# Performance work log

Measured on AMD Instinct MI355X. Metric: run time of the kernel, lower is better.

The kernel has to match this reference:

```python
import jax, jax.numpy as jnp
import numpy as np

MARGIN = 1.0


def _rand_offdiag(key, n):
    # uniform random index j != k for each row k (replaces Python random.choice)
    j = jax.random.randint(key, (n,), 0, n - 1)
    return j + (j >= jnp.arange(n)).astype(j.dtype)


def _semi_hard_margin_loss(logits, j_rand, j_fallback, margin):
    # logits: [N, N]; anchor for row k is logits[k, k]
    n = logits.shape[0]
    rows = jnp.arange(n)
    anchor = jnp.diagonal(logits)                      # [N]
    # term 1: random imposter, hinge at 0 (loss added only when diff > 0)
    imp1 = logits[rows, j_rand]
    d1 = jnp.maximum(imp1 - anchor + margin, 0.0)
    # term 2: semi-hard imposter = max over entries strictly below the anchor
    neg_inf = jnp.finfo(logits.dtype).min
    mask = logits < anchor[:, None]                    # diagonal never True
    cand_max = jnp.max(jnp.where(mask, logits, neg_inf), axis=1)
    has_cand = jnp.any(mask, axis=1)
    imp2 = jnp.where(has_cand, cand_max, logits[rows, j_fallback])
    d2 = jnp.maximum(imp2 - anchor + margin, 0.0)
    return jnp.mean(d1 + d2)


def setup_inputs() -> dict:
    key = jax.random.key(0)
    kx, ky = jax.random.split(key)
    x = jax.random.normal(kx, (4096, 1024), dtype=jnp.float32)
    y = jax.random.normal(ky, (4096, 1024), dtype=jnp.float32)
    return {"x": x, "y": y}


def reference(x, y):
    logits = jnp.matmul(x, y.T)                        # [N, N]
    n = logits.shape[0]
    k1, k2, k3, k4 = jax.random.split(jax.random.key(42), 4)
    loss = (_semi_hard_margin_loss(logits, _rand_offdiag(k1, n), _rand_offdiag(k2, n), MARGIN)
            + _semi_hard_margin_loss(logits.T, _rand_offdiag(k3, n), _rand_offdiag(k4, n), MARGIN))
    return loss
```

## Files before the change

### kernel.cpp

```cpp
#include <hip/hip_runtime.h>
#include <stdint.h>
#include <stddef.h>

#define NN 4096
#define KK 1024
#define SPAN 4095u

typedef unsigned short ushort_t;
typedef __attribute__((ext_vector_type(8))) short short8v;
typedef __attribute__((ext_vector_type(4))) float f32x4;

__host__ __device__ inline void tf2x32(uint32_t k0, uint32_t k1,
                                       uint32_t x0, uint32_t x1,
                                       uint32_t* o0, uint32_t* o1) {
  uint32_t ks2 = k0 ^ k1 ^ 0x1BD11BDAu;
  uint32_t v0 = x0 + k0;
  uint32_t v1 = x1 + k1;
#define TF_ROT(x, r) (((x) << (r)) | ((x) >> (32 - (r))))
#define TF_RND(r) do { v0 += v1; v1 = TF_ROT(v1, r); v1 ^= v0; } while (0)
  TF_RND(13); TF_RND(15); TF_RND(26); TF_RND(6);
  v0 += k1;  v1 += ks2 + 1u;
  TF_RND(17); TF_RND(29); TF_RND(16); TF_RND(24);
  v0 += ks2; v1 += k0 + 2u;
  TF_RND(13); TF_RND(15); TF_RND(26); TF_RND(6);
  v0 += k0;  v1 += k1 + 3u;
  TF_RND(17); TF_RND(29); TF_RND(16); TF_RND(24);
  v0 += k1;  v1 += ks2 + 4u;
  TF_RND(13); TF_RND(15); TF_RND(26); TF_RND(6);
  v0 += ks2; v1 += k0 + 5u;
#undef TF_RND
#undef TF_ROT
  *o0 = v0; *o1 = v1;
}

__device__ inline uint32_t rb32(uint32_t ka, uint32_t kb, uint32_t i) {
  uint32_t a, b;
  tf2x32(ka, kb, 0u, i, &a, &b);
  return a ^ b;
}

__device__ inline uint32_t fenc(float f) {
  uint32_t b = __float_as_uint(f);
  return (b & 0x80000000u) ? ~b : (b | 0x80000000u);
}
__device__ inline float fdec(uint32_t e) {
  uint32_t b = (e & 0x80000000u) ? (e & 0x7FFFFFFFu) : ~e;
  return __uint_as_float(b);
}

__device__ inline ushort_t bf16rne(float f) {
  uint32_t u = __float_as_uint(f);
  return (ushort_t)((u + 0x7FFFu + ((u >> 16) & 1u)) >> 16);
}

__device__ inline void glds16(const void* g, void* l) {
  __builtin_amdgcn_global_load_lds((const __attribute__((address_space(1))) void*)g,
                                   (__attribute__((address_space(3))) void*)l, 16, 0, 0);
}

template <int N> __device__ __forceinline__ void vmwait() {
  if constexpr (N == 8)      asm volatile("s_waitcnt vmcnt(8)" ::: "memory");
  else if constexpr (N == 4) asm volatile("s_waitcnt vmcnt(4)" ::: "memory");
  else                       asm volatile("s_waitcnt vmcnt(0)" ::: "memory");
}

__global__ __launch_bounds__(256) void k_prep(
    const float4* __restrict__ X, const float4* __restrict__ Y,
    ushort4* __restrict__ Xb, ushort4* __restrict__ Yb,
    uint32_t* __restrict__ rowmax, uint32_t* __restrict__ colmax) {
  const int b = blockIdx.x, tid = threadIdx.x;
  if (b < 16) rowmax[b * 256 + tid] = 0u;
  else if (b < 32) colmax[(b - 16) * 256 + tid] = 0u;
  const float4* src = (b < 2048) ? X : Y;
  ushort4* dst = (b < 2048) ? Xb : Yb;
  const int n4 = NN * KK / 4;
  for (int i = (b & 2047) * 256 + tid; i < n4; i += 2048 * 256) {
    float4 v = src[i];
    ushort4 o;
    o.x = bf16rne(v.x); o.y = bf16rne(v.y); o.z = bf16rne(v.z); o.w = bf16rne(v.w);
    dst[i] = o;
  }
}

__global__ __launch_bounds__(256) void k_dots(
    const float* __restrict__ X, const float* __restrict__ Y,
    uint32_t s0a, uint32_t s0b, uint32_t s1a, uint32_t s1b,
    uint32_t s2a, uint32_t s2b, uint32_t s3a, uint32_t s3b,
    float* __restrict__ anchor, float* __restrict__ irr, float* __restrict__ irf,
    float* __restrict__ icr, float* __restrict__ icf) {
  const int wid = threadIdx.x >> 6;
  const int lane = threadIdx.x & 63;
  const int row = blockIdx.x * 4 + wid;

  int jl = 0;
  if (lane < 4) {
    uint32_t ka = (lane == 0) ? s0a : (lane == 1) ? s1a : (lane == 2) ? s2a : s3a;
    uint32_t kb = (lane == 0) ? s0b : (lane == 1) ? s1b : (lane == 2) ? s2b : s3b;
    uint32_t k1a, k1b, k2a, k2b;
    tf2x32(ka, kb, 0u, 0u, &k1a, &k1b);
    tf2x32(ka, kb, 0u, 1u, &k2a, &k2b);
    uint32_t hi = rb32(k1a, k1b, (uint32_t)row);
    uint32_t lo = rb32(k2a, k2b, (uint32_t)row);
    uint32_t off = ((hi % SPAN) * 256u + (lo % SPAN)) % SPAN;
    int j = (int)off;
    jl = j + ((j >= row) ? 1 : 0);
  }
  const int j1r = __shfl(jl, 0), j1f = __shfl(jl, 1);
  const int j2r = __shfl(jl, 2), j2f = __shfl(jl, 3);

  const float4* xk = (const float4*)(X + (size_t)row * KK);
  const float4* yk = (const float4*)(Y + (size_t)row * KK);
  const float4* y1 = (const float4*)(Y + (size_t)j1r * KK);
  const float4* y2 = (const float4*)(Y + (size_t)j1f * KK);
  const float4* x1 = (const float4*)(X + (size_t)j2r * KK);
  const float4* x2 = (const float4*)(X + (size_t)j2f * KK);
  float sa = 0.f, s1 = 0.f, s2 = 0.f, s3 = 0.f, s4 = 0.f;
  for (int t = lane; t < KK / 4; t += 64) {
    float4 xv = xk[t], yv = yk[t], a1 = y1[t], a2 = y2[t], b1 = x1[t], b2 = x2[t];
    sa = fmaf(xv.x, yv.x, fmaf(xv.y, yv.y, fmaf(xv.z, yv.z, fmaf(xv.w, yv.w, sa))));
    s1 = fmaf(xv.x, a1.x, fmaf(xv.y, a1.y, fmaf(xv.z, a1.z, fmaf(xv.w, a1.w, s1))));
    s2 = fmaf(xv.x, a2.x, fmaf(xv.y, a2.y, fmaf(xv.z, a2.z, fmaf(xv.w, a2.w, s2))));
    s3 = fmaf(b1.x, yv.x, fmaf(b1.y, yv.y, fmaf(b1.z, yv.z, fmaf(b1.w, yv.w, s3))));
    s4 = fmaf(b2.x, yv.x, fmaf(b2.y, yv.y, fmaf(b2.z, yv.z, fmaf(b2.w, yv.w, s4))));
  }
  for (int m = 32; m >= 1; m >>= 1) {
    sa += __shfl_xor(sa, m);
    s1 += __shfl_xor(s1, m);
    s2 += __shfl_xor(s2, m);
    s3 += __shfl_xor(s3, m);
    s4 += __shfl_xor(s4, m);
  }
  if (lane == 0) {
    anchor[row] = sa; irr[row] = s1; irf[row] = s2; icr[row] = s3; icf[row] = s4;
  }
}

#define TBM 256
#define TBK 32
#define TNT (KK / TBK)

__global__ __launch_bounds__(512, 2) void k_gemm256(
    const ushort_t* __restrict__ A, const ushort_t* __restrict__ B,
    const float* __restrict__ anchor,
    uint32_t* __restrict__ rowmax, uint32_t* __restrict__ colmax) {
  __shared__ ushort_t Als[4][TBM * TBK];
  __shared__ ushort_t Bls[4][TBM * TBK];

  const int tid = threadIdx.x;
  const int lane = tid & 63;
  const int w = tid >> 6;
  const int wr = w >> 2, wc = w & 3;
  const int l15 = lane & 15, l4 = lane >> 4;

  const int swz = (blockIdx.x & 7) * 32 + (blockIdx.x >> 3);
  const int bi = swz >> 4, bj = swz & 15;

  const int sr = tid >> 2;
  const int ps = (tid & 3) ^ ((sr >> 1) & 3);
  const ushort_t* Ab0 = A + (size_t)(bi * TBM + sr) * KK + ps * 8;
  const ushort_t* Ab1 = Ab0 + (size_t)128 * KK;
  const ushort_t* Bb0 = B + (size_t)(bj * TBM + sr) * KK + ps * 8;
  const ushort_t* Bb1 = Bb0 + (size_t)128 * KK;

  int aoff[8], boff[4];
#pragma unroll
  for (int m = 0; m < 8; ++m) {
    int row = wr * 128 + m * 16 + l15;
    aoff[m] = row * TBK + ((l4 ^ ((row >> 1) & 3)) * 8);
  }
#pragma unroll
  for (int n = 0; n < 4; ++n) {
    int row = wc * 64 + n * 16 + l15;
    boff[n] = row * TBK + ((l4 ^ ((row >> 1) & 3)) * 8);
  }

  f32x4 acc[8][4] = {};

#define STAGE(SLOT, KKOFF)                                   \
  do {                                                       \
    glds16(Ab0 + (KKOFF), &Als[SLOT][tid * 8]);              \
    glds16(Ab1 + (KKOFF), &Als[SLOT][4096 + tid * 8]);       \
    glds16(Bb0 + (KKOFF), &Bls[SLOT][tid * 8]);              \
    glds16(Bb1 + (KKOFF), &Bls[SLOT][4096 + tid * 8]);       \
  } while (0)

#define GITER(T, VMN, DOSTAGE)                               \
  do {                                                       \
    vmwait<VMN>();                                           \
    __builtin_amdgcn_s_barrier();                            \
    asm volatile("" ::: "memory");                           \
    const int slot_ = (T) & 3;                               \
    if (DOSTAGE) STAGE(((T) + 3) & 3, ((T) + 3) * TBK);      \
    short8v bf[4];                                           \
    _Pragma("unroll")                                        \
    for (int n = 0; n < 4; ++n)                              \
      bf[n] = *(const short8v*)&Bls[slot_][boff[n]];         \
    __builtin_amdgcn_s_setprio(1);                           \
    _Pragma("unroll")                                        \
    for (int m = 0; m < 8; ++m) {                            \
      short8v am = *(const short8v*)&Als[slot_][aoff[m]];    \
      _Pragma("unroll")                                      \
      for (int n = 0; n < 4; ++n)                            \
        acc[m][n] = __builtin_amdgcn_mfma_f32_16x16x32_bf16( \
            am, bf[n], acc[m][n], 0, 0, 0);                  \
    }                                                        \
    __builtin_amdgcn_s_setprio(0);                           \
  } while (0)

  STAGE(0, 0);
  STAGE(1, TBK);
  STAGE(2, 2 * TBK);

  for (int t = 0; t < TNT - 3; ++t) GITER(t, 8, true);
  GITER(TNT - 3, 8, false);
  GITER(TNT - 2, 4, false);
  GITER(TNT - 1, 0, false);

#undef GITER
#undef STAGE

  const int rbase = bi * TBM + wr * 128;
  const int cbase = bj * TBM + wc * 64;

  float ar[32], ac[4];
#pragma unroll
  for (int m = 0; m < 8; ++m)
#pragma unroll
    for (int r = 0; r < 4; ++r)
      ar[m * 4 + r] = anchor[rbase + m * 16 + l4 * 4 + r];
#pragma unroll
  for (int n = 0; n < 4; ++n)
    ac[n] = anchor[cbase + n * 16 + l15];

#pragma unroll
  for (int m = 0; m < 8; ++m) {
#pragma unroll
    for (int r = 0; r < 4; ++r) {
      const int rg = rbase + m * 16 + l4 * 4 + r;
      const float a = ar[m * 4 + r];
      uint32_t e = 0;
#pragma unroll
      for (int n = 0; n < 4; ++n) {
        const int cg = cbase + n * 16 + l15;
        float v = acc[m][n][r];
        if (v < a && rg != cg) { uint32_t fe = fenc(v); e = (fe > e) ? fe : e; }
      }
#pragma unroll
      for (int sh = 1; sh < 16; sh <<= 1) {
        uint32_t o = (uint32_t)__shfl_xor((int)e, sh, 64);
        e = (o > e) ? o : e;
      }
      if (l15 == 0 && e) atomicMax(&rowmax[rg], e);
    }
  }
#pragma unroll
  for (int n = 0; n < 4; ++n) {
    const int cg = cbase + n * 16 + l15;
    const float a = ac[n];
    uint32_t e = 0;
#pragma unroll
    for (int m = 0; m < 8; ++m) {
#pragma unroll
      for (int r = 0; r < 4; ++r) {
        const int rg = rbase + m * 16 + l4 * 4 + r;
        float v = acc[m][n][r];
        if (v < a && rg != cg) { uint32_t fe = fenc(v); e = (fe > e) ? fe : e; }
      }
    }
    {
      uint32_t o = (uint32_t)__shfl_xor((int)e, 16, 64); e = (o > e) ? o : e;
      o = (uint32_t)__shfl_xor((int)e, 32, 64);          e = (o > e) ? o : e;
    }
    if (l4 == 0 && e) atomicMax(&colmax[cg], e);
  }
}

__global__ __launch_bounds__(256) void k_final(
    const float* __restrict__ anchor,
    const float* __restrict__ irr, const float* __restrict__ irf,
    const float* __restrict__ icr, const float* __restrict__ icf,
    const uint32_t* __restrict__ rowmax, const uint32_t* __restrict__ colmax,
    float* __restrict__ out) {
  float s = 0.f;
  for (int k = (int)threadIdx.x; k < NN; k += 256) {
    float a = anchor[k];
    float d1 = fmaxf(irr[k] - a + 1.0f, 0.f);
    uint32_t rm = rowmax[k];
    float imp2r = rm ? fdec(rm) : irf[k];
    float d2 = fmaxf(imp2r - a + 1.0f, 0.f);
    float e1 = fmaxf(icr[k] - a + 1.0f, 0.f);
    uint32_t cm = colmax[k];
    float imp2c = cm ? fdec(cm) : icf[k];
    float e2 = fmaxf(imp2c - a + 1.0f, 0.f);
    s += d1 + d2 + e1 + e2;
  }
  __shared__ float red[4];
  for (int m = 32; m >= 1; m >>= 1) s += __shfl_xor(s, m);
  if ((threadIdx.x & 63) == 0) red[threadIdx.x >> 6] = s;
  __syncthreads();
  if (threadIdx.x == 0) out[0] = (red[0] + red[1] + red[2] + red[3]) * (1.0f / NN);
}

extern "C" void kernel_launch(void* const* d_in, const int* in_sizes, int n_in,
                              void* d_out, int out_size, void* d_ws, size_t ws_size,
                              hipStream_t stream) {
  const float* X = (const float*)d_in[0];
  const float* Y = (const float*)d_in[1];
  float* out = (float*)d_out;

  char* ws = (char*)d_ws;
  float* anchor    = (float*)(ws + 0 * 16384);
  float* irr       = (float*)(ws + 1 * 16384);
  float* irf       = (float*)(ws + 2 * 16384);
  float* icr       = (float*)(ws + 3 * 16384);
  float* icf       = (float*)(ws + 4 * 16384);
  uint32_t* rowmax = (uint32_t*)(ws + 5 * 16384);
  uint32_t* colmax = (uint32_t*)(ws + 6 * 16384);
  ushort_t* Xb     = (ushort_t*)(ws + 256 * 1024);
  ushort_t* Yb     = Xb + (size_t)NN * KK;

  uint32_t sk[4][2];
  for (int i = 0; i < 4; ++i) tf2x32(0u, 42u, 0u, (uint32_t)i, &sk[i][0], &sk[i][1]);

  k_prep<<<4096, 256, 0, stream>>>((const float4*)X, (const float4*)Y,
                                   (ushort4*)Xb, (ushort4*)Yb, rowmax, colmax);

  k_dots<<<NN / 4, 256, 0, stream>>>(X, Y,
      sk[0][0], sk[0][1], sk[1][0], sk[1][1], sk[2][0], sk[2][1], sk[3][0], sk[3][1],
      anchor, irr, irf, icr, icf);

  k_gemm256<<<256, 512, 0, stream>>>(Xb, Yb, anchor, rowmax, colmax);

  k_final<<<1, 256, 0, stream>>>(anchor, irr, irf, icr, icf, rowmax, colmax, out);
}
```

Before: 103.0 us.

## Restructure GEMM main loop to double-buffered BK=64 with split interleaved staging

The bf16 GEMM mainloop moves from a 4-slot BK=32 ring with explicit vmcnt waits to a 2-buffer BK=64 scheme with an XOR swizzle over 8 column chunks. A and B global-to-LDS loads for the next tile are issued between MFMA sub-phases, and each iteration ends with a __syncthreads. The aim is to halve barrier count and interleave loads with MFMA work. The cost is shallower prefetch depth (one tile ahead instead of three) and a full barrier per iteration that includes the load drain, which could expose memory latency.

```diff
diff --git a/kernel.cpp b/kernel.cpp
--- a/kernel.cpp
+++ b/kernel.cpp
@@ -58,12 +58,6 @@
                                    (__attribute__((address_space(3))) void*)l, 16, 0, 0);
 }
 
-template <int N> __device__ __forceinline__ void vmwait() {
-  if constexpr (N == 8)      asm volatile("s_waitcnt vmcnt(8)" ::: "memory");
-  else if constexpr (N == 4) asm volatile("s_waitcnt vmcnt(4)" ::: "memory");
-  else                       asm volatile("s_waitcnt vmcnt(0)" ::: "memory");
-}
-
 __global__ __launch_bounds__(256) void k_prep(
     const float4* __restrict__ X, const float4* __restrict__ Y,
     ushort4* __restrict__ Xb, ushort4* __restrict__ Yb,
@@ -135,92 +129,111 @@
   }
 }
 
-#define TBM 256
-#define TBK 32
-#define TNT (KK / TBK)
 
 __global__ __launch_bounds__(512, 2) void k_gemm256(
     const ushort_t* __restrict__ A, const ushort_t* __restrict__ B,
     const float* __restrict__ anchor,
     uint32_t* __restrict__ rowmax, uint32_t* __restrict__ colmax) {
-  __shared__ ushort_t Als[4][TBM * TBK];
-  __shared__ ushort_t Bls[4][TBM * TBK];
+  __shared__ ushort_t AL[2][256 * 64];
+  __shared__ ushort_t BL[2][256 * 64];
 
   const int tid = threadIdx.x;
   const int lane = tid & 63;
-  const int w = tid >> 6;
-  const int wr = w >> 2, wc = w & 3;
+  const int w = tid >> 6, wr = w >> 2, wc = w & 3;
   const int l15 = lane & 15, l4 = lane >> 4;
 
   const int swz = (blockIdx.x & 7) * 32 + (blockIdx.x >> 3);
   const int bi = swz >> 4, bj = swz & 15;
 
-  const int sr = tid >> 2;
-  const int ps = (tid & 3) ^ ((sr >> 1) & 3);
-  const ushort_t* Ab0 = A + (size_t)(bi * TBM + sr) * KK + ps * 8;
-  const ushort_t* Ab1 = Ab0 + (size_t)128 * KK;
-  const ushort_t* Bb0 = B + (size_t)(bj * TBM + sr) * KK + ps * 8;
-  const ushort_t* Bb1 = Bb0 + (size_t)128 * KK;
-
-  int aoff[8], boff[4];
-#pragma unroll
-  for (int m = 0; m < 8; ++m) {
-    int row = wr * 128 + m * 16 + l15;
-    aoff[m] = row * TBK + ((l4 ^ ((row >> 1) & 3)) * 8);
-  }
-#pragma unroll
-  for (int n = 0; n < 4; ++n) {
-    int row = wc * 64 + n * 16 + l15;
-    boff[n] = row * TBK + ((l4 ^ ((row >> 1) & 3)) * 8);
-  }
+  const int strow = tid >> 3;
+  const int scol = ((tid & 7) ^ (strow & 7)) * 8;
+  const ushort_t* Asrc = A + (size_t)(bi * 256 + strow) * KK + scol;
+  const ushort_t* Bsrc = B + (size_t)(bj * 256 + strow) * KK + scol;
+
+  const int arow0 = wr * 128 + l15;
+  const int brow0 = wc * 64 + l15;
+  const int ap0 = ((l4) ^ (l15 & 7)) * 8;
+  const int ap1 = ((4 + l4) ^ (l15 & 7)) * 8;
 
   f32x4 acc[8][4] = {};
 
-#define STAGE(SLOT, KKOFF)                                   \
-  do {                                                       \
-    glds16(Ab0 + (KKOFF), &Als[SLOT][tid * 8]);              \
-    glds16(Ab1 + (KKOFF), &Als[SLOT][4096 + tid * 8]);       \
-    glds16(Bb0 + (KKOFF), &Bls[SLOT][tid * 8]);              \
-    glds16(Bb1 + (KKOFF), &Bls[SLOT][4096 + tid * 8]);       \
-  } while (0)
-
-#define GITER(T, VMN, DOSTAGE)                               \
-  do {                                                       \
-    vmwait<VMN>();                                           \
-    __builtin_amdgcn_s_barrier();                            \
-    asm volatile("" ::: "memory");                           \
-    const int slot_ = (T) & 3;                               \
-    if (DOSTAGE) STAGE(((T) + 3) & 3, ((T) + 3) * TBK);      \
-    short8v bf[4];                                           \
-    _Pragma("unroll")                                        \
-    for (int n = 0; n < 4; ++n)                              \
-      bf[n] = *(const short8v*)&Bls[slot_][boff[n]];         \
-    __builtin_amdgcn_s_setprio(1);                           \
-    _Pragma("unroll")                                        \
-    for (int m = 0; m < 8; ++m) {                            \
-      short8v am = *(const short8v*)&Als[slot_][aoff[m]];    \
-      _Pragma("unroll")                                      \
-      for (int n = 0; n < 4; ++n)                            \
-        acc[m][n] = __builtin_amdgcn_mfma_f32_16x16x32_bf16( \
-            am, bf[n], acc[m][n], 0, 0, 0);                  \
-    }                                                        \
-    __builtin_amdgcn_s_setprio(0);                           \
-  } while (0)
-
-  STAGE(0, 0);
-  STAGE(1, TBK);
-  STAGE(2, 2 * TBK);
-
-  for (int t = 0; t < TNT - 3; ++t) GITER(t, 8, true);
-  GITER(TNT - 3, 8, false);
-  GITER(TNT - 2, 4, false);
-  GITER(TNT - 1, 0, false);
-
-#undef GITER
-#undef STAGE
-
-  const int rbase = bi * TBM + wr * 128;
-  const int cbase = bj * TBM + wc * 64;
+#define MFMA16(a, b, c) __builtin_amdgcn_mfma_f32_16x16x32_bf16(a, b, c, 0, 0, 0)
+
+#pragma unroll
+  for (int i = 0; i < 4; ++i)
+    glds16(Asrc + (size_t)i * 64 * KK, &AL[0][tid * 8 + i * 4096]);
+#pragma unroll
+  for (int i = 0; i < 4; ++i)
+    glds16(Bsrc + (size_t)i * 64 * KK, &BL[0][tid * 8 + i * 4096]);
+  __syncthreads();
+
+  for (int t = 0; t < 16; ++t) {
+    const int buf = t & 1, nxt = buf ^ 1;
+    const size_t kk = (size_t)(t + 1) * 64;
+    short8v af[8], b0, b1;
+
+    if (t < 15) {
+#pragma unroll
+      for (int i = 0; i < 4; ++i)
+        glds16(Asrc + (size_t)i * 64 * KK + kk, &AL[nxt][tid * 8 + i * 4096]);
+    }
+#pragma unroll
+    for (int m = 0; m < 8; ++m)
+      af[m] = *(const short8v*)&AL[buf][(arow0 + m * 16) * 64 + ap0];
+    b0 = *(const short8v*)&BL[buf][(brow0) * 64 + ap0];
+    b1 = *(const short8v*)&BL[buf][(brow0 + 16) * 64 + ap0];
+    __builtin_amdgcn_s_setprio(1);
+#pragma unroll
+    for (int m = 0; m < 8; ++m) {
+      acc[m][0] = MFMA16(af[m], b0, acc[m][0]);
+      acc[m][1] = MFMA16(af[m], b1, acc[m][1]);
+    }
+    __builtin_amdgcn_s_setprio(0);
+
+    if (t < 15) {
+#pragma unroll
+      for (int i = 0; i < 4; ++i)
+        glds16(Bsrc + (size_t)i * 64 * KK + kk, &BL[nxt][tid * 8 + i * 4096]);
+    }
+    b0 = *(const short8v*)&BL[buf][(brow0 + 32) * 64 + ap0];
+    b1 = *(const short8v*)&BL[buf][(brow0 + 48) * 64 + ap0];
+    __builtin_amdgcn_s_setprio(1);
+#pragma unroll
+    for (int m = 0; m < 8; ++m) {
+      acc[m][2] = MFMA16(af[m], b0, acc[m][2]);
+      acc[m][3] = MFMA16(af[m], b1, acc[m][3]);
+    }
+    __builtin_amdgcn_s_setprio(0);
+
+#pragma unroll
+    for (int m = 0; m < 8; ++m)
+      af[m] = *(const short8v*)&AL[buf][(arow0 + m * 16) * 64 + ap1];
+    b0 = *(const short8v*)&BL[buf][(brow0) * 64 + ap1];
+    b1 = *(const short8v*)&BL[buf][(brow0 + 16) * 64 + ap1];
+    __builtin_amdgcn_s_setprio(1);
+#pragma unroll
+    for (int m = 0; m < 8; ++m) {
+      acc[m][0] = MFMA16(af[m], b0, acc[m][0]);
+      acc[m][1] = MFMA16(af[m], b1, acc[m][1]);
+    }
+    __builtin_amdgcn_s_setprio(0);
+
+    b0 = *(const short8v*)&BL[buf][(brow0 + 32) * 64 + ap1];
+    b1 = *(const short8v*)&BL[buf][(brow0 + 48) * 64 + ap1];
+    __builtin_amdgcn_s_setprio(1);
+#pragma unroll
+    for (int m = 0; m < 8; ++m) {
+      acc[m][2] = MFMA16(af[m], b0, acc[m][2]);
+      acc[m][3] = MFMA16(af[m], b1, acc[m][3]);
+    }
+    __builtin_amdgcn_s_setprio(0);
+
+    __syncthreads();
+  }
+#undef MFMA16
+
+  const int rbase = bi * 256 + wr * 128;
+  const int cbase = bj * 256 + wc * 64;
 
   float ar[32], ac[4];
 #pragma unroll
```

Measured after the change: 99.88 us. -3.1%, faster.

## Replace 256x256 four-stage GEMM with 128x128 double-buffered tile kernel

Applied to the files above, without the earlier changes.

Swaps the 512-thread, 256x256-tile GEMM (four-stage LDS pipeline, swizzled layout, explicit vmcnt waits) for a 256-thread, 128x128-tile kernel with two LDS buffers and plain __syncthreads. The grid grows from 256 to 1024 blocks for more parallelism and a shorter tail, and the pipeline code gets simpler. In exchange, tile reuse drops, the unswizzled LDS layout risks bank conflicts, and each iteration ends in a full barrier with little prefetch depth.

```diff
diff --git a/kernel.cpp b/kernel.cpp
--- a/kernel.cpp
+++ b/kernel.cpp
@@ -58,12 +58,6 @@
                                    (__attribute__((address_space(3))) void*)l, 16, 0, 0);
 }
 
-template <int N> __device__ __forceinline__ void vmwait() {
-  if constexpr (N == 8)      asm volatile("s_waitcnt vmcnt(8)" ::: "memory");
-  else if constexpr (N == 4) asm volatile("s_waitcnt vmcnt(4)" ::: "memory");
-  else                       asm volatile("s_waitcnt vmcnt(0)" ::: "memory");
-}
-
 __global__ __launch_bounds__(256) void k_prep(
     const float4* __restrict__ X, const float4* __restrict__ Y,
     ushort4* __restrict__ Xb, ushort4* __restrict__ Yb,
@@ -135,96 +129,65 @@
   }
 }
 
-#define TBM 256
-#define TBK 32
-#define TNT (KK / TBK)
-
-__global__ __launch_bounds__(512, 2) void k_gemm256(
+
+__global__ __launch_bounds__(256, 2) void k_gemm97(
     const ushort_t* __restrict__ A, const ushort_t* __restrict__ B,
     const float* __restrict__ anchor,
     uint32_t* __restrict__ rowmax, uint32_t* __restrict__ colmax) {
-  __shared__ ushort_t Als[4][TBM * TBK];
-  __shared__ ushort_t Bls[4][TBM * TBK];
+  __shared__ ushort_t AL[2][4096];
+  __shared__ ushort_t BL[2][4096];
 
   const int tid = threadIdx.x;
   const int lane = tid & 63;
-  const int w = tid >> 6;
-  const int wr = w >> 2, wc = w & 3;
+  const int w = tid >> 6, wr = w >> 1, wc = w & 1;
   const int l15 = lane & 15, l4 = lane >> 4;
 
-  const int swz = (blockIdx.x & 7) * 32 + (blockIdx.x >> 3);
-  const int bi = swz >> 4, bj = swz & 15;
-
-  const int sr = tid >> 2;
-  const int ps = (tid & 3) ^ ((sr >> 1) & 3);
-  const ushort_t* Ab0 = A + (size_t)(bi * TBM + sr) * KK + ps * 8;
-  const ushort_t* Ab1 = Ab0 + (size_t)128 * KK;
-  const ushort_t* Bb0 = B + (size_t)(bj * TBM + sr) * KK + ps * 8;
-  const ushort_t* Bb1 = Bb0 + (size_t)128 * KK;
-
-  int aoff[8], boff[4];
-#pragma unroll
-  for (int m = 0; m < 8; ++m) {
-    int row = wr * 128 + m * 16 + l15;
-    aoff[m] = row * TBK + ((l4 ^ ((row >> 1) & 3)) * 8);
-  }
-#pragma unroll
-  for (int n = 0; n < 4; ++n) {
-    int row = wc * 64 + n * 16 + l15;
-    boff[n] = row * TBK + ((l4 ^ ((row >> 1) & 3)) * 8);
-  }
-
-  f32x4 acc[8][4] = {};
-
-#define STAGE(SLOT, KKOFF)                                   \
-  do {                                                       \
-    glds16(Ab0 + (KKOFF), &Als[SLOT][tid * 8]);              \
-    glds16(Ab1 + (KKOFF), &Als[SLOT][4096 + tid * 8]);       \
-    glds16(Bb0 + (KKOFF), &Bls[SLOT][tid * 8]);              \
-    glds16(Bb1 + (KKOFF), &Bls[SLOT][4096 + tid * 8]);       \
-  } while (0)
-
-#define GITER(T, VMN, DOSTAGE)                               \
-  do {                                                       \
-    vmwait<VMN>();                                           \
-    __builtin_amdgcn_s_barrier();                            \
-    asm volatile("" ::: "memory");                           \
-    const int slot_ = (T) & 3;                               \
-    if (DOSTAGE) STAGE(((T) + 3) & 3, ((T) + 3) * TBK);      \
-    short8v bf[4];                                           \
-    _Pragma("unroll")                                        \
-    for (int n = 0; n < 4; ++n)                              \
-      bf[n] = *(const short8v*)&Bls[slot_][boff[n]];         \
-    __builtin_amdgcn_s_setprio(1);                           \
-    _Pragma("unroll")                                        \
-    for (int m = 0; m < 8; ++m) {                            \
-      short8v am = *(const short8v*)&Als[slot_][aoff[m]];    \
-      _Pragma("unroll")                                      \
-      for (int n = 0; n < 4; ++n)                            \
-        acc[m][n] = __builtin_amdgcn_mfma_f32_16x16x32_bf16( \
-            am, bf[n], acc[m][n], 0, 0, 0);                  \
-    }                                                        \
-    __builtin_amdgcn_s_setprio(0);                           \
-  } while (0)
-
-  STAGE(0, 0);
-  STAGE(1, TBK);
-  STAGE(2, 2 * TBK);
-
-  for (int t = 0; t < TNT - 3; ++t) GITER(t, 8, true);
-  GITER(TNT - 3, 8, false);
-  GITER(TNT - 2, 4, false);
-  GITER(TNT - 1, 0, false);
-
-#undef GITER
-#undef STAGE
-
-  const int rbase = bi * TBM + wr * 128;
-  const int cbase = bj * TBM + wc * 64;
-
-  float ar[32], ac[4];
-#pragma unroll
-  for (int m = 0; m < 8; ++m)
+  const int swz = (blockIdx.x & 7) * 128 + (blockIdx.x >> 3);
+  const int bi = swz >> 5, bj = swz & 31;
+
+  const int strow = tid >> 2, scol = (tid & 3) * 8;
+  const ushort_t* Asrc = A + (size_t)(bi * 128 + strow) * KK + scol;
+  const ushort_t* Bsrc = B + (size_t)(bj * 128 + strow) * KK + scol;
+
+  const int aoff = (wr * 64 + l15) * 32 + l4 * 8;
+  const int boff = (wc * 64 + l15) * 32 + l4 * 8;
+
+  f32x4 acc[4][4] = {};
+
+  glds16(Asrc,           &AL[0][tid * 8]);
+  glds16(Asrc + 64 * KK, &AL[0][2048 + tid * 8]);
+  glds16(Bsrc,           &BL[0][tid * 8]);
+  glds16(Bsrc + 64 * KK, &BL[0][2048 + tid * 8]);
+  __syncthreads();
+
+  for (int t = 0; t < 32; ++t) {
+    const int buf = t & 1;
+    if (t < 31) {
+      const size_t kk = (size_t)(t + 1) * 32;
+      glds16(Asrc + kk,           &AL[buf ^ 1][tid * 8]);
+      glds16(Asrc + 64 * KK + kk, &AL[buf ^ 1][2048 + tid * 8]);
+      glds16(Bsrc + kk,           &BL[buf ^ 1][tid * 8]);
+      glds16(Bsrc + 64 * KK + kk, &BL[buf ^ 1][2048 + tid * 8]);
+    }
+    short8v af[4], bf[4];
+#pragma unroll
+    for (int m = 0; m < 4; ++m) af[m] = *(const short8v*)&AL[buf][aoff + m * 512];
+#pragma unroll
+    for (int n = 0; n < 4; ++n) bf[n] = *(const short8v*)&BL[buf][boff + n * 512];
+#pragma unroll
+    for (int m = 0; m < 4; ++m)
+#pragma unroll
+      for (int n = 0; n < 4; ++n)
+        acc[m][n] = __builtin_amdgcn_mfma_f32_16x16x32_bf16(af[m], bf[n], acc[m][n], 0, 0, 0);
+    __syncthreads();
+  }
+
+  const int rbase = bi * 128 + wr * 64;
+  const int cbase = bj * 128 + wc * 64;
+
+  float ar[16], ac[4];
+#pragma unroll
+  for (int m = 0; m < 4; ++m)
 #pragma unroll
     for (int r = 0; r < 4; ++r)
       ar[m * 4 + r] = anchor[rbase + m * 16 + l4 * 4 + r];
@@ -233,7 +196,7 @@
     ac[n] = anchor[cbase + n * 16 + l15];
 
 #pragma unroll
-  for (int m = 0; m < 8; ++m) {
+  for (int m = 0; m < 4; ++m) {
 #pragma unroll
     for (int r = 0; r < 4; ++r) {
       const int rg = rbase + m * 16 + l4 * 4 + r;
@@ -259,7 +222,7 @@
     const float a = ac[n];
     uint32_t e = 0;
 #pragma unroll
-    for (int m = 0; m < 8; ++m) {
+    for (int m = 0; m < 4; ++m) {
 #pragma unroll
       for (int r = 0; r < 4; ++r) {
         const int rg = rbase + m * 16 + l4 * 4 + r;
@@ -329,7 +292,7 @@
       sk[0][0], sk[0][1], sk[1][0], sk[1][1], sk[2][0], sk[2][1], sk[3][0], sk[3][1],
       anchor, irr, irf, icr, icf);
 
-  k_gemm256<<<256, 512, 0, stream>>>(Xb, Yb, anchor, rowmax, colmax);
+  k_gemm97<<<1024, 256, 0, stream>>>(Xb, Yb, anchor, rowmax, colmax);
 
   k_final<<<1, 256, 0, stream>>>(anchor, irr, irf, icr, icf, rowmax, colmax, out);
 }
```

Measured after the change: 105.5 us. 1.02x slower.
